# Optimization experiments

Hardware: AMD Instinct MI355X
Metric: run time of the kernel (lower is better)

## Reference

```python
import jax, jax.numpy as jnp
import numpy as np

B = 8192
HID = 1024
VD = 1024
NH = 16
DH = HID // NH  # 64
TOPK = 8
LN_EPS = 1e-5


def setup_inputs() -> dict:
    key = jax.random.key(0)
    ks = jax.random.split(key, 10)
    s = 1.0 / np.sqrt(HID)
    return {
        "hidden_state": jax.random.normal(ks[0], (B, HID), dtype=jnp.float32),
        "memory_keys": jax.random.normal(ks[1], (B, TOPK, HID), dtype=jnp.float32),
        "memory_values": jax.random.normal(ks[2], (B, TOPK, VD), dtype=jnp.float32),
        "Wq": jax.random.normal(ks[3], (HID, HID), dtype=jnp.float32) * s,
        "Wk": jax.random.normal(ks[4], (HID, HID), dtype=jnp.float32) * s,
        "Wv": jax.random.normal(ks[5], (VD, HID), dtype=jnp.float32) * s,
        "Wo": jax.random.normal(ks[6], (HID, HID), dtype=jnp.float32) * s,
        "Wg": jax.random.normal(ks[7], (2 * HID, HID), dtype=jnp.float32) * s,
        "bg": jnp.zeros((HID,), dtype=jnp.float32),
        "ln_g": jnp.ones((HID,), dtype=jnp.float32),
        "ln_b": jnp.zeros((HID,), dtype=jnp.float32),
    }


def reference(hidden_state, memory_keys, memory_values, Wq, Wk, Wv, Wo, Wg, bg, ln_g, ln_b):
    b = hidden_state.shape[0]
    scale = DH ** -0.5
    # QKV projections, reshaped into heads
    Q = (hidden_state @ Wq).reshape(b, NH, DH)          # (B, H, D)
    K = (memory_keys @ Wk).reshape(b, TOPK, NH, DH)     # (B, K, H, D)
    V = (memory_values @ Wv).reshape(b, TOPK, NH, DH)   # (B, K, H, D)
    # attention over top_k memory slots (query length 1)
    scores = jnp.einsum("bhd,bkhd->bhk", Q, K) * scale  # (B, H, K)
    attn = jax.nn.softmax(scores, axis=-1)
    out = jnp.einsum("bhk,bkhd->bhd", attn, V).reshape(b, HID)
    memory_out = out @ Wo
    # gated residual
    gate_in = jnp.concatenate([hidden_state, memory_out], axis=-1)
    g = jax.nn.sigmoid(gate_in @ Wg + bg)
    aug = hidden_state + g * memory_out
    # LayerNorm (affine, eps=1e-5)
    mean = jnp.mean(aug, axis=-1, keepdims=True)
    var = jnp.var(aug, axis=-1, keepdims=True)
    return (aug - mean) * jax.lax.rsqrt(var + LN_EPS) * ln_g + ln_b
```

## Files before the change

kernel.cpp:

```cpp
#include <hip/hip_runtime.h>
#include <hip/hip_bf16.h>

typedef __bf16 bf16;
typedef __bf16 bf16x8 __attribute__((ext_vector_type(8)));
typedef __bf16 bf16x4 __attribute__((ext_vector_type(4)));
typedef float  f32x4  __attribute__((ext_vector_type(4)));

__device__ __forceinline__ void block_barrier()
{
    asm volatile("s_waitcnt lgkmcnt(0)\n\ts_barrier" ::: "memory");
}

#if defined(__has_builtin)
#if __has_builtin(__builtin_amdgcn_global_load_lds)
#define HAS_GLD 1
#endif
#endif
#ifndef HAS_GLD
#define HAS_GLD 0
#endif

__device__ __forceinline__ void gld_lds16(const bf16* g, bf16* lds_base)
{
#if HAS_GLD
    __builtin_amdgcn_global_load_lds(
        (const __attribute__((address_space(1))) void*)g,
        (__attribute__((address_space(3))) void*)lds_base, 16, 0, 0);
#else
    *(bf16x8*)(lds_base + (threadIdx.x & 63) * 8) = *(const bf16x8*)g;
#endif
}

__global__ __launch_bounds__(256)
void transpose_cvt(const float* __restrict__ src, bf16* __restrict__ dst, int K, int N)
{
    __shared__ float t[32][33];
    const int bx = blockIdx.x, by = blockIdx.y, tid = threadIdx.x;
    const int c = tid & 31, r0 = tid >> 5;
#pragma unroll
    for (int p = 0; p < 4; p++) {
        int r = r0 + p * 8;
        t[r][c] = src[(size_t)(by * 32 + r) * N + bx * 32 + c];
    }
    __syncthreads();
#pragma unroll
    for (int p = 0; p < 4; p++) {
        int r = r0 + p * 8;
        dst[(size_t)(bx * 32 + r) * K + by * 32 + c] = (bf16)t[c][r];
    }
}

__global__ __launch_bounds__(256)
void cvt_bf16(const float* __restrict__ src, bf16* __restrict__ dst, int n8)
{
    const int i = blockIdx.x * 256 + threadIdx.x;
    if (i >= n8) return;
    const float4* s = (const float4*)(src + (size_t)i * 8);
    float4 a = s[0], b = s[1];
    bf16x8 o;
    o[0] = (bf16)a.x; o[1] = (bf16)a.y; o[2] = (bf16)a.z; o[3] = (bf16)a.w;
    o[4] = (bf16)b.x; o[5] = (bf16)b.y; o[6] = (bf16)b.z; o[7] = (bf16)b.w;
    *(bf16x8*)(dst + (size_t)i * 8) = o;
}

__global__ __launch_bounds__(256)
void repack_wv(const bf16* __restrict__ Wvt, bf16* __restrict__ Wvf)
{
    const int t = blockIdx.x * 256 + threadIdx.x;
    const int lane = t & 63, g = t >> 6;
    const int dt = g & 3, sp = (g >> 2) & 31, h = g >> 7;
    const int lm = lane & 15, q = lane >> 4;
    const bf16x8 v = *(const bf16x8*)(Wvt + (size_t)(h * 64 + dt * 16 + lm) * 1024
                                      + sp * 32 + q * 8);
    *(bf16x8*)(Wvf + (size_t)g * 512 + lane * 8) = v;
}

__global__ __launch_bounds__(256)
void repack_q(const bf16* __restrict__ Qb, bf16* __restrict__ Qf)
{
    const int t = blockIdx.x * 256 + threadIdx.x;
    const int lane = t & 63, g = t >> 6;
    const int half = g & 1, h = (g >> 1) & 15, bt = g >> 5;
    const int lm = lane & 15, q = lane >> 4;
    const bf16x8 v = *(const bf16x8*)(Qb + (size_t)(bt * 16 + lm) * 1024
                                      + h * 64 + half * 32 + q * 8);
    *(bf16x8*)(Qf + (size_t)g * 512 + lane * 8) = v;
}

__global__ __launch_bounds__(256)
void repack_wk2(const bf16* __restrict__ Wkb, bf16* __restrict__ Wkf)
{
    const int t = blockIdx.x * 256 + threadIdx.x;
    const int lane = t & 63, g = t >> 6;
    const int half = g & 1, h = (g >> 1) & 15, mt = (g >> 5) & 1, sp = g >> 6;
    const int lm = lane & 15, q = lane >> 4;
    const bf16x8 v = *(const bf16x8*)(Wkb + (size_t)(sp * 32 + mt * 16 + lm) * 1024
                                      + h * 64 + half * 32 + q * 8);
    *(bf16x8*)(Wkf + (size_t)g * 512 + lane * 8) = v;
}

template<bool TWOA>
__global__ __launch_bounds__(256)
void gemm_a97(const bf16* __restrict__ A1, const bf16* __restrict__ A2,
              const bf16* __restrict__ Bt, float* __restrict__ Cf,
              bf16* __restrict__ Cb, int Kloop, int Ksplit,
              int ldA, int ldA2, int ldB, int ldC,
              long az, long bz, long cz)
{
    __shared__ bf16 Al[128 * 32];
    __shared__ bf16 Bl[128 * 32];

    const int z = blockIdx.z;
    A1 += (size_t)z * az;
    Bt += (size_t)z * bz;
    if (Cf) Cf += (size_t)z * cz;
    if (Cb) Cb += (size_t)z * cz;

    int bx, by;
    {
        const int gy = gridDim.y;
        const int flat = blockIdx.y * gridDim.x + blockIdx.x;
        if ((gy & 7) == 0 && gridDim.x == 8) {
            const int xcd = flat & 7, slot = flat >> 3, mpx = gy >> 3;
            by = xcd * mpx + (slot >> 3);
            bx = slot & 7;
        } else { bx = blockIdx.x; by = blockIdx.y; }
    }

    const int tid = threadIdx.x;
    const int wave = tid >> 6, lane = tid & 63;
    const int m0 = by * 128, n0 = bx * 128;
    const int rl = lane >> 2;
    const int kc = (lane & 3) * 8;
    const int wm = wave >> 1, wn = wave & 1, lm = lane & 15, quad = lane >> 4;

    f32x4 acc[4][4];
#pragma unroll
    for (int i = 0; i < 4; i++)
#pragma unroll
        for (int j = 0; j < 4; j++)
#pragma unroll
            for (int r = 0; r < 4; r++) acc[i][j][r] = 0.f;

    for (int k0 = 0; k0 < Kloop; k0 += 32) {
        const bf16* Ab; int kof, ld;
        if (TWOA && k0 >= Ksplit) { Ab = A2; kof = k0 - Ksplit; ld = ldA2; }
        else                      { Ab = A1; kof = k0;          ld = ldA;  }
        const int r0 = wave * 32 + rl, r1 = r0 + 16;
        gld_lds16(Ab + (size_t)(m0 + r0) * ld + kof + kc, Al + (wave * 32) * 32);
        gld_lds16(Ab + (size_t)(m0 + r1) * ld + kof + kc, Al + (wave * 32 + 16) * 32);
        gld_lds16(Bt + (size_t)(n0 + r0) * ldB + k0 + kc, Bl + (wave * 32) * 32);
        gld_lds16(Bt + (size_t)(n0 + r1) * ldB + k0 + kc, Bl + (wave * 32 + 16) * 32);
        __syncthreads();

        bf16x8 af[4], bfr[4];
#pragma unroll
        for (int i = 0; i < 4; i++)
            af[i] = *(const bf16x8*)&Al[(wm * 64 + i * 16 + lm) * 32 + quad * 8];
#pragma unroll
        for (int j = 0; j < 4; j++)
            bfr[j] = *(const bf16x8*)&Bl[(wn * 64 + j * 16 + lm) * 32 + quad * 8];
#pragma unroll
        for (int i = 0; i < 4; i++)
#pragma unroll
            for (int j = 0; j < 4; j++)
                acc[i][j] = __builtin_amdgcn_mfma_f32_16x16x32_bf16(af[i], bfr[j], acc[i][j], 0, 0, 0);
        __syncthreads();
    }

#pragma unroll
    for (int i = 0; i < 4; i++) {
        const int rbase = m0 + wm * 64 + i * 16 + quad * 4;
#pragma unroll
        for (int j = 0; j < 4; j++) {
            const int c = n0 + wn * 64 + j * 16 + lm;
#pragma unroll
            for (int r = 0; r < 4; r++) {
                const float v = acc[i][j][r];
                const size_t idx = (size_t)(rbase + r) * ldC + c;
                if (Cf) Cf[idx] = v;
                if (Cb) Cb[idx] = (bf16)v;
            }
        }
    }
}

__global__ __launch_bounds__(512, 4)
void score_attn(const bf16* __restrict__ Qf, const bf16* __restrict__ Wkf,
                const float* __restrict__ mk, float* __restrict__ attn)
{
    __shared__ bf16  Ul[16 * 16 * 32];
    __shared__ float Ml[2][4096];

    const int tid  = threadIdx.x;
    const int wave = tid >> 6, lane = tid & 63;
    const int lm = lane & 15, q = lane >> 4;
    const int bt = blockIdx.x;
    const int h0 = wave * 2;

    const int gk = lane & 7, gg4 = lane >> 3;

    bf16x8 qf[2][2];
#pragma unroll
    for (int hh = 0; hh < 2; hh++)
#pragma unroll
        for (int half = 0; half < 2; half++)
            qf[hh][half] = *(const bf16x8*)(Qf +
                (size_t)((bt * 16 + h0 + hh) * 2 + half) * 512 + lane * 8);

    f32x4 sacc[2];
#pragma unroll
    for (int lb = 0; lb < 2; lb++)
#pragma unroll
        for (int r = 0; r < 4; r++) sacc[lb][r] = 0.f;

#pragma unroll
    for (int m = 0; m < 2; m++) {
        const int row = 2 * wave + m;
        gld_lds16((const bf16*)(mk + (size_t)(bt * 16 + row) * 8192 + gk * 1024 + gg4 * 4),
                  (bf16*)&Ml[0][row * 256]);
    }

    for (int sp = 0; sp < 32; ++sp) {
        const int ni = (sp + 1 < 32) ? (sp + 1) * 32 : 0;
        const int cb = sp & 1, nb = cb ^ 1;

        bf16x8 wk[2][2][2];
#pragma unroll
        for (int hh = 0; hh < 2; hh++)
#pragma unroll
            for (int mt = 0; mt < 2; mt++)
#pragma unroll
                for (int half = 0; half < 2; half++)
                    wk[hh][mt][half] = *(const bf16x8*)(Wkf +
                        (size_t)(((sp * 2 + mt) * 16 + h0 + hh) * 2 + half) * 512 + lane * 8);
        __builtin_amdgcn_sched_barrier(0);

#pragma unroll
        for (int m = 0; m < 2; m++) {
            const int row = 2 * wave + m;
            gld_lds16((const bf16*)(mk + (size_t)(bt * 16 + row) * 8192 + gk * 1024 + ni + gg4 * 4),
                      (bf16*)&Ml[nb][row * 256]);
        }
        __builtin_amdgcn_sched_barrier(0);

        asm volatile("s_waitcnt vmcnt(2)" ::: "memory");
        __builtin_amdgcn_sched_barrier(0);
#pragma unroll
        for (int hh = 0; hh < 2; hh++) {
            const int h = h0 + hh;
#pragma unroll
            for (int mt = 0; mt < 2; mt++) {
                f32x4 c4;
                c4[0] = 0.f; c4[1] = 0.f; c4[2] = 0.f; c4[3] = 0.f;
                c4 = __builtin_amdgcn_mfma_f32_16x16x32_bf16(wk[hh][mt][0], qf[hh][0], c4, 0, 0, 0);
                c4 = __builtin_amdgcn_mfma_f32_16x16x32_bf16(wk[hh][mt][1], qf[hh][1], c4, 0, 0, 0);
                bf16x4 o;
                o[0] = (bf16)c4[0]; o[1] = (bf16)c4[1]; o[2] = (bf16)c4[2]; o[3] = (bf16)c4[3];
                *(bf16x4*)((char*)Ul + ((((lm * 16 + h) * 32 + mt * 16 + q * 4) * 2)
                                        ^ (((lm ^ h) & 7) << 4))) = o;
            }
        }
        block_barrier();

#pragma unroll
        for (int lb = 0; lb < 2; lb++) {
            const int bb = wave * 2 + lb;
            const bf16x8 ua = *(const bf16x8*)((char*)Ul +
                ((((bb * 16 + lm) * 32 + q * 8) * 2) ^ (((bb ^ lm) & 7) << 4)));
            const int mbase = bb * 256 + (lane & 7) * 4;
            (void)mbase;
            const int kk = lm & 7;
            const f32x4 a0 = *(const f32x4*)&Ml[cb][bb * 256 + (q * 2) * 32 + kk * 4];
            const f32x4 a1 = *(const f32x4*)&Ml[cb][bb * 256 + (q * 2 + 1) * 32 + kk * 4];
            bf16x8 mb;
            mb[0] = (bf16)a0[0]; mb[1] = (bf16)a0[1]; mb[2] = (bf16)a0[2]; mb[3] = (bf16)a0[3];
            mb[4] = (bf16)a1[0]; mb[5] = (bf16)a1[1]; mb[6] = (bf16)a1[2]; mb[7] = (bf16)a1[3];
            sacc[lb] = __builtin_amdgcn_mfma_f32_16x16x32_bf16(ua, mb, sacc[lb], 0, 0, 0);
        }
        block_barrier();
    }

#pragma unroll
    for (int lb = 0; lb < 2; lb++) {
        const size_t bb = (size_t)(bt * 16 + wave * 2 + lb);
#pragma unroll
        for (int r = 0; r < 4; r++) {
            float s = sacc[lb][r] * 0.125f;
            float mx = s;
            mx = fmaxf(mx, __shfl_xor(mx, 1));
            mx = fmaxf(mx, __shfl_xor(mx, 2));
            mx = fmaxf(mx, __shfl_xor(mx, 4));
            mx = fmaxf(mx, __shfl_xor(mx, 8));
            const float e = __expf(s - mx);
            float d = e;
            d += __shfl_xor(d, 1);
            d += __shfl_xor(d, 2);
            d += __shfl_xor(d, 4);
            d += __shfl_xor(d, 8);
            const float a = e * (2.f / d);
            if (lm < 8) attn[bb * 128 + (q * 4 + r) * 8 + lm] = a;
        }
    }
}

__global__ __launch_bounds__(512, 4)
void apply_attn(const float* __restrict__ attn, const float* __restrict__ mv,
                const bf16* __restrict__ Wvf, bf16* __restrict__ OH)
{
    __shared__ float Vl32[3][4096];
    __shared__ bf16  Wl[16 * 16 * 32];

    const int tid  = threadIdx.x;
    const int wave = tid >> 6, lane = tid & 63;
    const int lm = lane & 15, q = lane >> 4;
    const int b0 = blockIdx.x * 16;
    const int h0 = wave * 2;

    const int gk = lane >> 3, gi4 = (lane & 7) * 4;

    bf16x8 afv[2][2];
#pragma unroll
    for (int lb = 0; lb < 2; lb++) {
        const float* ap = attn + (size_t)(b0 + wave * 2 + lb) * 128 + lm * 8;
        const float4 x = *(const float4*)(ap);
        const float4 y = *(const float4*)(ap + 4);
        bf16 a8[8];
        a8[0] = (bf16)x.x; a8[1] = (bf16)x.y; a8[2] = (bf16)x.z; a8[3] = (bf16)x.w;
        a8[4] = (bf16)y.x; a8[5] = (bf16)y.y; a8[6] = (bf16)y.z; a8[7] = (bf16)y.w;
#pragma unroll
        for (int mt = 0; mt < 2; mt++) {
            bf16x8 t;
#pragma unroll
            for (int j = 0; j < 8; j++) t[j] = (q == mt) ? a8[j] : (bf16)0.f;
            afv[lb][mt] = t;
        }
    }

    f32x4 oacc[2][4];
#pragma unroll
    for (int i = 0; i < 2; i++)
#pragma unroll
        for (int j = 0; j < 4; j++)
#pragma unroll
            for (int r = 0; r < 4; r++) oacc[i][j][r] = 0.f;

#pragma unroll
    for (int m = 0; m < 2; m++) {
        const int row = 2 * wave + m;
        gld_lds16((const bf16*)(mv + (size_t)(b0 + row) * 8192 + gk * 1024 + gi4),
                  (bf16*)&Vl32[0][row * 256]);
    }
#pragma unroll
    for (int m = 0; m < 2; m++) {
        const int row = 2 * wave + m;
        gld_lds16((const bf16*)(mv + (size_t)(b0 + row) * 8192 + gk * 1024 + 32 + gi4),
                  (bf16*)&Vl32[1][row * 256]);
    }

    for (int sp = 0; sp < 32; ++sp) {
        const int ni = (sp + 2 < 32) ? sp * 32 + 64 : 0;
        const int cb = sp % 3, nb = (sp + 2) % 3;

        bf16x8 wb[2][4];
#pragma unroll
        for (int hh = 0; hh < 2; hh++) {
            const int h = h0 + hh;
#pragma unroll
            for (int dt = 0; dt < 4; dt++)
                wb[hh][dt] = *(const bf16x8*)(Wvf +
                    ((((size_t)h * 32 + sp) * 4 + dt) * 512 + lane * 8));
        }
        __builtin_amdgcn_sched_barrier(0);

#pragma unroll
        for (int m = 0; m < 2; m++) {
            const int row = 2 * wave + m;
            gld_lds16((const bf16*)(mv + (size_t)(b0 + row) * 8192 + gk * 1024 + ni + gi4),
                      (bf16*)&Vl32[nb][row * 256]);
        }
        __builtin_amdgcn_sched_barrier(0);

        asm volatile("s_waitcnt vmcnt(12)" ::: "memory");
        __builtin_amdgcn_sched_barrier(0);
#pragma unroll
        for (int lb = 0; lb < 2; lb++) {
            const int row = 2 * wave + lb;
            const int il = (q & 1) * 16 + lm;
            float v[8];
#pragma unroll
            for (int k = 0; k < 8; k++) v[k] = Vl32[cb][row * 256 + k * 32 + il];
            bf16x8 avf;
#pragma unroll
            for (int k = 0; k < 8; k++) avf[k] = (bf16)v[k];
#pragma unroll
            for (int mt = 0; mt < 2; mt++) {
                f32x4 c;
                c[0] = 0.f; c[1] = 0.f; c[2] = 0.f; c[3] = 0.f;
                c = __builtin_amdgcn_mfma_f32_16x16x32_bf16(avf, afv[lb][mt], c, 0, 0, 0);
                bf16x4 o;
                o[0] = (bf16)c[0]; o[1] = (bf16)c[1]; o[2] = (bf16)c[2]; o[3] = (bf16)c[3];
                *(bf16x4*)((char*)Wl + ((((row * 16 + lm) * 32 + mt * 16 + q * 4) * 2)
                                        ^ (((row ^ lm) & 7) << 4))) = o;
            }
        }
        block_barrier();

        asm volatile("s_waitcnt vmcnt(2)" ::: "memory");
        __builtin_amdgcn_sched_barrier(0);
#pragma unroll
        for (int hh = 0; hh < 2; hh++) {
            const int h = h0 + hh;
            const bf16x8 wa = *(const bf16x8*)((char*)Wl +
                ((((lm * 16 + h) * 32 + q * 8) * 2) ^ (((lm ^ h) & 7) << 4)));
#pragma unroll
            for (int dt = 0; dt < 4; dt++)
                oacc[hh][dt] = __builtin_amdgcn_mfma_f32_16x16x32_bf16(wa, wb[hh][dt], oacc[hh][dt], 0, 0, 0);
        }
        block_barrier();
    }

#pragma unroll
    for (int hh = 0; hh < 2; hh++) {
        const int h = h0 + hh;
#pragma unroll
        for (int dt = 0; dt < 4; dt++) {
#pragma unroll
            for (int r = 0; r < 4; r++)
                OH[(size_t)(b0 + q * 4 + r) * 1024 + h * 64 + dt * 16 + lm] = (bf16)oacc[hh][dt][r];
        }
    }
}

__global__ __launch_bounds__(256)
void gate_ln_kernel(const float* __restrict__ hs, const float* __restrict__ mo,
                    const float* __restrict__ z,  const float* __restrict__ bg,
                    const float* __restrict__ lng, const float* __restrict__ lnb,
                    float* __restrict__ out)
{
    __shared__ float s1[4], s2[4];
    const int tid = threadIdx.x;
    const size_t base = (size_t)blockIdx.x * 1024 + tid * 4;

    const float4 h4 = *(const float4*)&hs[base];
    const float4 m4 = *(const float4*)&mo[base];
    const float4 z4 = *(const float4*)&z[base];
    const float4 bg4 = *(const float4*)&bg[tid * 4];

    float a[4];
    {
        const float g0 = 1.f / (1.f + __expf(-(z4.x + bg4.x)));
        const float g1 = 1.f / (1.f + __expf(-(z4.y + bg4.y)));
        const float g2 = 1.f / (1.f + __expf(-(z4.z + bg4.z)));
        const float g3 = 1.f / (1.f + __expf(-(z4.w + bg4.w)));
        a[0] = h4.x + g0 * m4.x;
        a[1] = h4.y + g1 * m4.y;
        a[2] = h4.z + g2 * m4.z;
        a[3] = h4.w + g3 * m4.w;
    }
    float sum = a[0] + a[1] + a[2] + a[3];
    float sq  = a[0]*a[0] + a[1]*a[1] + a[2]*a[2] + a[3]*a[3];
#pragma unroll
    for (int off = 32; off >= 1; off >>= 1) {
        sum += __shfl_xor(sum, off);
        sq  += __shfl_xor(sq,  off);
    }
    const int wave = tid >> 6;
    if ((tid & 63) == 0) { s1[wave] = sum; s2[wave] = sq; }
    __syncthreads();
    const float mean = (s1[0] + s1[1] + s1[2] + s1[3]) * (1.f / 1024.f);
    const float var  = (s2[0] + s2[1] + s2[2] + s2[3]) * (1.f / 1024.f) - mean * mean;
    const float inv  = rsqrtf(var + 1e-5f);

    const float4 g4 = *(const float4*)&lng[tid * 4];
    const float4 b4 = *(const float4*)&lnb[tid * 4];
    float4 o;
    o.x = (a[0] - mean) * inv * g4.x + b4.x;
    o.y = (a[1] - mean) * inv * g4.y + b4.y;
    o.z = (a[2] - mean) * inv * g4.z + b4.z;
    o.w = (a[3] - mean) * inv * g4.w + b4.w;
    *(float4*)&out[base] = o;
}

extern "C" void kernel_launch(void* const* d_in, const int* in_sizes, int n_in,
                              void* d_out, int out_size, void* d_ws, size_t ws_size,
                              hipStream_t stream)
{
    const float* hs  = (const float*)d_in[0];
    const float* mk  = (const float*)d_in[1];
    const float* mv  = (const float*)d_in[2];
    const float* Wq  = (const float*)d_in[3];
    const float* Wk  = (const float*)d_in[4];
    const float* Wv  = (const float*)d_in[5];
    const float* Wo  = (const float*)d_in[6];
    const float* Wg  = (const float*)d_in[7];
    const float* bg  = (const float*)d_in[8];
    const float* lng = (const float*)d_in[9];
    const float* lnb = (const float*)d_in[10];
    float* out = (float*)d_out;

    const int B = 8192;
    const dim3 tb(256);

    char* ws = (char*)d_ws;
    bf16*  Wq_t = (bf16*)(ws);
    bf16*  Wv_t = (bf16*)(ws + ((size_t)2  << 20));
    bf16*  Wo_t = (bf16*)(ws + ((size_t)4  << 20));
    bf16*  Wg_t = (bf16*)(ws + ((size_t)6  << 20));
    bf16*  Wk_b = (bf16*)(ws + ((size_t)10 << 20));
    bf16*  hs_b = (bf16*)(ws + ((size_t)12 << 20));
    bf16*  Qb   = (bf16*)(ws + ((size_t)28 << 20));
    bf16*  OH   = (bf16*)(ws + ((size_t)44 << 20));
    float* Mo   = (float*)(ws + ((size_t)60 << 20));
    bf16*  Mo_b = (bf16*)(ws + ((size_t)92 << 20));
    float* Zb   = (float*)(ws + ((size_t)108 << 20));
    float* At   = (float*)(ws + ((size_t)140 << 20));
    bf16*  Wvf  = (bf16*)(ws + ((size_t)208 << 20));
    bf16*  Wkf  = (bf16*)(ws + ((size_t)210 << 20));
    bf16*  Qf   = (bf16*)(ws + ((size_t)212 << 20));

    transpose_cvt<<<dim3(32, 32), tb, 0, stream>>>(Wq, Wq_t, 1024, 1024);
    transpose_cvt<<<dim3(32, 32), tb, 0, stream>>>(Wv, Wv_t, 1024, 1024);
    transpose_cvt<<<dim3(32, 32), tb, 0, stream>>>(Wo, Wo_t, 1024, 1024);
    transpose_cvt<<<dim3(32, 64), tb, 0, stream>>>(Wg, Wg_t, 2048, 1024);
    cvt_bf16<<<dim3(1024 * 1024 / 8 / 256), tb, 0, stream>>>(Wk, Wk_b, 1024 * 1024 / 8);
    cvt_bf16<<<dim3(B * 1024 / 8 / 256), tb, 0, stream>>>(hs, hs_b, B * 1024 / 8);
    repack_wv<<<dim3(512), tb, 0, stream>>>(Wv_t, Wvf);
    repack_wk2<<<dim3(512), tb, 0, stream>>>(Wk_b, Wkf);

    gemm_a97<false><<<dim3(8, 64, 1), tb, 0, stream>>>(
        hs_b, nullptr, Wq_t, nullptr, Qb,
        1024, 1024, 1024, 0, 1024, 1024, 0, 0, 0);
    repack_q<<<dim3(4096), tb, 0, stream>>>(Qb, Qf);
    score_attn<<<dim3(B / 16), dim3(512), 0, stream>>>(Qf, Wkf, mk, At);
    apply_attn<<<dim3(B / 16), dim3(512), 0, stream>>>(At, mv, Wvf, OH);
    gemm_a97<false><<<dim3(8, 64, 1), tb, 0, stream>>>(
        OH, nullptr, Wo_t, Mo, Mo_b,
        1024, 1024, 1024, 0, 1024, 1024, 0, 0, 0);
    gemm_a97<true><<<dim3(8, 64, 1), tb, 0, stream>>>(
        hs_b, Mo_b, Wg_t, Zb, nullptr,
        2048, 1024, 1024, 1024, 2048, 1024, 0, 0, 0);
    gate_ln_kernel<<<dim3(B), tb, 0, stream>>>(
        hs, Mo, Zb, bg, lng, lnb, out);
}
```

Before: 426.3 us.

## Prefetch next-step weight fragments into ping-pong registers in score and apply kernels

Both the score and apply_attn loops now load the weight fragments for the following step into a second register set (ping-pong A/B buffers) while computing with the current set, so the global weight loads are no longer exposed at the start of each step. apply_attn drops its triple-buffered LDS staging of memory values in favour of double buffering, freeing shared memory. The vmcnt waits are retuned to match the new count of in-flight loads. The extra register sets raise VGPR pressure, which may reduce occupancy, and the shallower LDS pipeline in apply_attn leaves less latency slack for the memory-value loads.

```diff
diff --git a/kernel.cpp b/kernel.cpp
--- a/kernel.cpp
+++ b/kernel.cpp
@@ -214,6 +214,16 @@
 #pragma unroll
         for (int r = 0; r < 4; r++) sacc[lb][r] = 0.f;
 
+    bf16x8 wkA[2][2][2], wkB[2][2][2];
+
+#pragma unroll
+    for (int hh = 0; hh < 2; hh++)
+#pragma unroll
+        for (int mt = 0; mt < 2; mt++)
+#pragma unroll
+            for (int half = 0; half < 2; half++)
+                wkA[hh][mt][half] = *(const bf16x8*)(Wkf +
+                    (size_t)(((0 * 2 + mt) * 16 + h0 + hh) * 2 + half) * 512 + lane * 8);
 #pragma unroll
     for (int m = 0; m < 2; m++) {
         const int row = 2 * wave + m;
@@ -221,65 +231,69 @@
                   (bf16*)&Ml[0][row * 256]);
     }
 
-    for (int sp = 0; sp < 32; ++sp) {
-        const int ni = (sp + 1 < 32) ? (sp + 1) * 32 : 0;
-        const int cb = sp & 1, nb = cb ^ 1;
-
-        bf16x8 wk[2][2][2];
-#pragma unroll
-        for (int hh = 0; hh < 2; hh++)
-#pragma unroll
-            for (int mt = 0; mt < 2; mt++)
-#pragma unroll
-                for (int half = 0; half < 2; half++)
-                    wk[hh][mt][half] = *(const bf16x8*)(Wkf +
-                        (size_t)(((sp * 2 + mt) * 16 + h0 + hh) * 2 + half) * 512 + lane * 8);
-        __builtin_amdgcn_sched_barrier(0);
-
-#pragma unroll
-        for (int m = 0; m < 2; m++) {
-            const int row = 2 * wave + m;
-            gld_lds16((const bf16*)(mk + (size_t)(bt * 16 + row) * 8192 + gk * 1024 + ni + gg4 * 4),
-                      (bf16*)&Ml[nb][row * 256]);
-        }
-        __builtin_amdgcn_sched_barrier(0);
-
-        asm volatile("s_waitcnt vmcnt(2)" ::: "memory");
-        __builtin_amdgcn_sched_barrier(0);
-#pragma unroll
-        for (int hh = 0; hh < 2; hh++) {
-            const int h = h0 + hh;
-#pragma unroll
-            for (int mt = 0; mt < 2; mt++) {
-                f32x4 c4;
-                c4[0] = 0.f; c4[1] = 0.f; c4[2] = 0.f; c4[3] = 0.f;
-                c4 = __builtin_amdgcn_mfma_f32_16x16x32_bf16(wk[hh][mt][0], qf[hh][0], c4, 0, 0, 0);
-                c4 = __builtin_amdgcn_mfma_f32_16x16x32_bf16(wk[hh][mt][1], qf[hh][1], c4, 0, 0, 0);
-                bf16x4 o;
-                o[0] = (bf16)c4[0]; o[1] = (bf16)c4[1]; o[2] = (bf16)c4[2]; o[3] = (bf16)c4[3];
-                *(bf16x4*)((char*)Ul + ((((lm * 16 + h) * 32 + mt * 16 + q * 4) * 2)
-                                        ^ (((lm ^ h) & 7) << 4))) = o;
-            }
-        }
-        block_barrier();
-
-#pragma unroll
-        for (int lb = 0; lb < 2; lb++) {
-            const int bb = wave * 2 + lb;
-            const bf16x8 ua = *(const bf16x8*)((char*)Ul +
-                ((((bb * 16 + lm) * 32 + q * 8) * 2) ^ (((bb ^ lm) & 7) << 4)));
-            const int mbase = bb * 256 + (lane & 7) * 4;
-            (void)mbase;
-            const int kk = lm & 7;
-            const f32x4 a0 = *(const f32x4*)&Ml[cb][bb * 256 + (q * 2) * 32 + kk * 4];
-            const f32x4 a1 = *(const f32x4*)&Ml[cb][bb * 256 + (q * 2 + 1) * 32 + kk * 4];
-            bf16x8 mb;
-            mb[0] = (bf16)a0[0]; mb[1] = (bf16)a0[1]; mb[2] = (bf16)a0[2]; mb[3] = (bf16)a0[3];
-            mb[4] = (bf16)a1[0]; mb[5] = (bf16)a1[1]; mb[6] = (bf16)a1[2]; mb[7] = (bf16)a1[3];
-            sacc[lb] = __builtin_amdgcn_mfma_f32_16x16x32_bf16(ua, mb, sacc[lb], 0, 0, 0);
-        }
-        block_barrier();
-    }
+#define SCORE_STEP(SP, CUR, NXT) do {                                         \
+    const int nspf = ((SP) + 1 < 32) ? (SP) + 1 : 0;                          \
+    const int ni_  = nspf * 32;                                               \
+    const int nb_  = ((SP) + 1) & 1, cb_ = (SP) & 1;                          \
+                           \
+    _Pragma("unroll")                                                         \
+    for (int hh = 0; hh < 2; hh++)                                            \
+        _Pragma("unroll")                                                     \
+        for (int mt = 0; mt < 2; mt++)                                        \
+            _Pragma("unroll")                                                 \
+            for (int half = 0; half < 2; half++)                              \
+                NXT[hh][mt][half] = *(const bf16x8*)(Wkf +                    \
+                    (size_t)(((nspf * 2 + mt) * 16 + h0 + hh) * 2 + half) * 512 + lane * 8); \
+    __builtin_amdgcn_sched_barrier(0);                                        \
+                                 \
+    _Pragma("unroll")                                                         \
+    for (int m = 0; m < 2; m++) {                                             \
+        const int row = 2 * wave + m;                                         \
+        gld_lds16((const bf16*)(mk + (size_t)(bt * 16 + row) * 8192 + gk * 1024 + ni_ + gg4 * 4), \
+                  (bf16*)&Ml[nb_][row * 256]);                                \
+    }                                                                         \
+    __builtin_amdgcn_sched_barrier(0);                                        \
+           \
+    asm volatile("s_waitcnt vmcnt(10)" ::: "memory");                         \
+    __builtin_amdgcn_sched_barrier(0);                                        \
+                                                 \
+    _Pragma("unroll")                                                         \
+    for (int hh = 0; hh < 2; hh++) {                                          \
+        const int h = h0 + hh;                                                \
+        _Pragma("unroll")                                                     \
+        for (int mt = 0; mt < 2; mt++) {                                      \
+            f32x4 c4; c4[0] = 0.f; c4[1] = 0.f; c4[2] = 0.f; c4[3] = 0.f;     \
+            c4 = __builtin_amdgcn_mfma_f32_16x16x32_bf16(CUR[hh][mt][0], qf[hh][0], c4, 0, 0, 0); \
+            c4 = __builtin_amdgcn_mfma_f32_16x16x32_bf16(CUR[hh][mt][1], qf[hh][1], c4, 0, 0, 0); \
+            bf16x4 o;                                                         \
+            o[0] = (bf16)c4[0]; o[1] = (bf16)c4[1]; o[2] = (bf16)c4[2]; o[3] = (bf16)c4[3]; \
+            *(bf16x4*)((char*)Ul + ((((lm * 16 + h) * 32 + mt * 16 + q * 4) * 2) \
+                                    ^ (((lm ^ h) & 7) << 4))) = o;            \
+        }                                                                     \
+    }                                                                         \
+    block_barrier();                    \
+                             \
+    _Pragma("unroll")                                                         \
+    for (int lb = 0; lb < 2; lb++) {                                          \
+        const int bb = wave * 2 + lb;                                         \
+        const bf16x8 ua = *(const bf16x8*)((char*)Ul +                        \
+            ((((bb * 16 + lm) * 32 + q * 8) * 2) ^ (((bb ^ lm) & 7) << 4)));  \
+        const int kk = lm & 7;                                                \
+        const f32x4 a0 = *(const f32x4*)&Ml[cb_][bb * 256 + (q * 2) * 32 + kk * 4]; \
+        const f32x4 a1 = *(const f32x4*)&Ml[cb_][bb * 256 + (q * 2 + 1) * 32 + kk * 4]; \
+        bf16x8 mb;                                                            \
+        mb[0] = (bf16)a0[0]; mb[1] = (bf16)a0[1]; mb[2] = (bf16)a0[2]; mb[3] = (bf16)a0[3]; \
+        mb[4] = (bf16)a1[0]; mb[5] = (bf16)a1[1]; mb[6] = (bf16)a1[2]; mb[7] = (bf16)a1[3]; \
+        sacc[lb] = __builtin_amdgcn_mfma_f32_16x16x32_bf16(ua, mb, sacc[lb], 0, 0, 0); \
+    }                                                                         \
+    block_barrier();                               \
+} while (0)
+
+    for (int t = 0; t < 16; ++t) {
+        SCORE_STEP(2 * t,     wkA, wkB);
+        SCORE_STEP(2 * t + 1, wkB, wkA);
+    }
+#undef SCORE_STEP
 
 #pragma unroll
     for (int lb = 0; lb < 2; lb++) {
@@ -308,7 +322,7 @@
 void apply_attn(const float* __restrict__ attn, const float* __restrict__ mv,
                 const bf16* __restrict__ Wvf, bf16* __restrict__ OH)
 {
-    __shared__ float Vl32[3][4096];
+    __shared__ float Vl32[2][4096];
     __shared__ bf16  Wl[16 * 16 * 32];
 
     const int tid  = threadIdx.x;
@@ -345,80 +359,88 @@
 #pragma unroll
             for (int r = 0; r < 4; r++) oacc[i][j][r] = 0.f;
 
+    bf16x8 wbA[2][4], wbB[2][4];
+
+#pragma unroll
+    for (int hh = 0; hh < 2; hh++) {
+        const int h = h0 + hh;
+#pragma unroll
+        for (int dt = 0; dt < 4; dt++)
+            wbA[hh][dt] = *(const bf16x8*)(Wvf +
+                ((((size_t)h * 32 + 0) * 4 + dt) * 512 + lane * 8));
+    }
 #pragma unroll
     for (int m = 0; m < 2; m++) {
         const int row = 2 * wave + m;
         gld_lds16((const bf16*)(mv + (size_t)(b0 + row) * 8192 + gk * 1024 + gi4),
                   (bf16*)&Vl32[0][row * 256]);
     }
-#pragma unroll
-    for (int m = 0; m < 2; m++) {
-        const int row = 2 * wave + m;
-        gld_lds16((const bf16*)(mv + (size_t)(b0 + row) * 8192 + gk * 1024 + 32 + gi4),
-                  (bf16*)&Vl32[1][row * 256]);
-    }
-
-    for (int sp = 0; sp < 32; ++sp) {
-        const int ni = (sp + 2 < 32) ? sp * 32 + 64 : 0;
-        const int cb = sp % 3, nb = (sp + 2) % 3;
-
-        bf16x8 wb[2][4];
-#pragma unroll
-        for (int hh = 0; hh < 2; hh++) {
-            const int h = h0 + hh;
-#pragma unroll
-            for (int dt = 0; dt < 4; dt++)
-                wb[hh][dt] = *(const bf16x8*)(Wvf +
-                    ((((size_t)h * 32 + sp) * 4 + dt) * 512 + lane * 8));
-        }
-        __builtin_amdgcn_sched_barrier(0);
-
-#pragma unroll
-        for (int m = 0; m < 2; m++) {
-            const int row = 2 * wave + m;
-            gld_lds16((const bf16*)(mv + (size_t)(b0 + row) * 8192 + gk * 1024 + ni + gi4),
-                      (bf16*)&Vl32[nb][row * 256]);
-        }
-        __builtin_amdgcn_sched_barrier(0);
-
-        asm volatile("s_waitcnt vmcnt(12)" ::: "memory");
-        __builtin_amdgcn_sched_barrier(0);
-#pragma unroll
-        for (int lb = 0; lb < 2; lb++) {
-            const int row = 2 * wave + lb;
-            const int il = (q & 1) * 16 + lm;
-            float v[8];
-#pragma unroll
-            for (int k = 0; k < 8; k++) v[k] = Vl32[cb][row * 256 + k * 32 + il];
-            bf16x8 avf;
-#pragma unroll
-            for (int k = 0; k < 8; k++) avf[k] = (bf16)v[k];
-#pragma unroll
-            for (int mt = 0; mt < 2; mt++) {
-                f32x4 c;
-                c[0] = 0.f; c[1] = 0.f; c[2] = 0.f; c[3] = 0.f;
-                c = __builtin_amdgcn_mfma_f32_16x16x32_bf16(avf, afv[lb][mt], c, 0, 0, 0);
-                bf16x4 o;
-                o[0] = (bf16)c[0]; o[1] = (bf16)c[1]; o[2] = (bf16)c[2]; o[3] = (bf16)c[3];
-                *(bf16x4*)((char*)Wl + ((((row * 16 + lm) * 32 + mt * 16 + q * 4) * 2)
-                                        ^ (((row ^ lm) & 7) << 4))) = o;
-            }
-        }
-        block_barrier();
-
-        asm volatile("s_waitcnt vmcnt(2)" ::: "memory");
-        __builtin_amdgcn_sched_barrier(0);
-#pragma unroll
-        for (int hh = 0; hh < 2; hh++) {
-            const int h = h0 + hh;
-            const bf16x8 wa = *(const bf16x8*)((char*)Wl +
-                ((((lm * 16 + h) * 32 + q * 8) * 2) ^ (((lm ^ h) & 7) << 4)));
-#pragma unroll
-            for (int dt = 0; dt < 4; dt++)
-                oacc[hh][dt] = __builtin_amdgcn_mfma_f32_16x16x32_bf16(wa, wb[hh][dt], oacc[hh][dt], 0, 0, 0);
-        }
-        block_barrier();
-    }
+
+#define APPLY_STEP(SP, CUR, NXT) do {                                         \
+    const int nspf = ((SP) + 1 < 32) ? (SP) + 1 : 0;                          \
+    const int ni_  = nspf * 32;                                               \
+    const int nb_  = ((SP) + 1) & 1, cb_ = (SP) & 1;                          \
+                           \
+    _Pragma("unroll")                                                         \
+    for (int hh = 0; hh < 2; hh++) {                                          \
+        const int h = h0 + hh;                                                \
+        _Pragma("unroll")                                                     \
+        for (int dt = 0; dt < 4; dt++)                                        \
+            NXT[hh][dt] = *(const bf16x8*)(Wvf +                              \
+                ((((size_t)h * 32 + nspf) * 4 + dt) * 512 + lane * 8));       \
+    }                                                                         \
+    __builtin_amdgcn_sched_barrier(0);                                        \
+                            \
+    _Pragma("unroll")                                                         \
+    for (int m = 0; m < 2; m++) {                                             \
+        const int row = 2 * wave + m;                                         \
+        gld_lds16((const bf16*)(mv + (size_t)(b0 + row) * 8192 + gk * 1024 + ni_ + gi4), \
+                  (bf16*)&Vl32[nb_][row * 256]);                              \
+    }                                                                         \
+    __builtin_amdgcn_sched_barrier(0);                                        \
+          \
+    asm volatile("s_waitcnt vmcnt(10)" ::: "memory");                         \
+    __builtin_amdgcn_sched_barrier(0);                                        \
+                               \
+    _Pragma("unroll")                                                         \
+    for (int lb = 0; lb < 2; lb++) {                                          \
+        const int row = 2 * wave + lb;                                        \
+        const int il = (q & 1) * 16 + lm;                                     \
+        float v[8];                                                           \
+        _Pragma("unroll")                                                     \
+        for (int k = 0; k < 8; k++) v[k] = Vl32[cb_][row * 256 + k * 32 + il]; \
+        bf16x8 avf;                                                           \
+        _Pragma("unroll")                                                     \
+        for (int k = 0; k < 8; k++) avf[k] = (bf16)v[k];                      \
+        _Pragma("unroll")                                                     \
+        for (int mt = 0; mt < 2; mt++) {                                      \
+            f32x4 c; c[0] = 0.f; c[1] = 0.f; c[2] = 0.f; c[3] = 0.f;          \
+            c = __builtin_amdgcn_mfma_f32_16x16x32_bf16(avf, afv[lb][mt], c, 0, 0, 0); \
+            bf16x4 o;                                                         \
+            o[0] = (bf16)c[0]; o[1] = (bf16)c[1]; o[2] = (bf16)c[2]; o[3] = (bf16)c[3]; \
+            *(bf16x4*)((char*)Wl + ((((row * 16 + lm) * 32 + mt * 16 + q * 4) * 2) \
+                                    ^ (((row ^ lm) & 7) << 4))) = o;          \
+        }                                                                     \
+    }                                                                         \
+    block_barrier();                    \
+                                           \
+    _Pragma("unroll")                                                         \
+    for (int hh = 0; hh < 2; hh++) {                                          \
+        const int h = h0 + hh;                                                \
+        const bf16x8 wa = *(const bf16x8*)((char*)Wl +                        \
+            ((((lm * 16 + h) * 32 + q * 8) * 2) ^ (((lm ^ h) & 7) << 4)));    \
+        _Pragma("unroll")                                                     \
+        for (int dt = 0; dt < 4; dt++)                                        \
+            oacc[hh][dt] = __builtin_amdgcn_mfma_f32_16x16x32_bf16(wa, CUR[hh][dt], oacc[hh][dt], 0, 0, 0); \
+    }                                                                         \
+    block_barrier();                                         \
+} while (0)
+
+    for (int t = 0; t < 16; ++t) {
+        APPLY_STEP(2 * t,     wbA, wbB);
+        APPLY_STEP(2 * t + 1, wbB, wbA);
+    }
+#undef APPLY_STEP
 
 #pragma unroll
     for (int hh = 0; hh < 2; hh++) {
```

New measurement: 526.4 us. +23.5%, slower.
